# Kernel optimization log

Hardware: AMD Instinct MI355X
Metric: run time of the kernel (lower is better)

Reference implementation:

```python
import jax, jax.numpy as jnp
import numpy as np

# ---- fixed heterogeneous-graph metadata (Hetionet-like) ----
N_C, N_D, N_G = 15000, 3000, 40000          # Compound, Disease, Gene node counts
NODE_N = [N_C, N_D, N_G]
HID, OUT, HEADS, LAYERS = 128, 64, 4, 2
DH = HID // HEADS                            # 32 = head dim
# edge types as (src_type, dst_type):
#  0 treats C->D, 1 rev_treats D->C, 2 binds C->G, 3 rev_binds G->C, 4 interacts G->G
EDGE_META = [(0, 1), (1, 0), (0, 2), (2, 0), (2, 2)]
E_CNT = [80000, 80000, 250000, 250000, 400000]
N_EDGE_TYPES = len(EDGE_META)
N_ADD = 8000                                 # int(n_train * ratio * (epoch-1)) = int(80000*0.05*2)


def setup_inputs() -> dict:
    key = jax.random.key(0)
    ks = iter(jax.random.split(key, 64))
    s = 0.05
    inp = {}
    # node-type embedding tables (the model uses embed.weight as input features)
    inp['emb_compound'] = jax.random.normal(next(ks), (N_C, HID), jnp.float32) * s
    inp['emb_disease'] = jax.random.normal(next(ks), (N_D, HID), jnp.float32) * s
    inp['emb_gene'] = jax.random.normal(next(ks), (N_G, HID), jnp.float32) * s
    # HGTConv params, stacked over [layer, node_type] / [layer, edge_type]
    inp['W_kqv'] = jax.random.normal(next(ks), (LAYERS, 3, HID, 3 * HID), jnp.float32) * s
    inp['b_kqv'] = jnp.zeros((LAYERS, 3, 3 * HID), jnp.float32)
    inp['W_out'] = jax.random.normal(next(ks), (LAYERS, 3, HID, HID), jnp.float32) * s
    inp['b_out'] = jnp.zeros((LAYERS, 3, HID), jnp.float32)
    inp['skip'] = jnp.ones((LAYERS, 3), jnp.float32)
    inp['a_rel'] = jax.random.normal(next(ks), (LAYERS, N_EDGE_TYPES, HEADS, DH, DH), jnp.float32) * s
    inp['m_rel'] = jax.random.normal(next(ks), (LAYERS, N_EDGE_TYPES, HEADS, DH, DH), jnp.float32) * s
    inp['p_rel'] = jnp.ones((LAYERS, N_EDGE_TYPES, HEADS), jnp.float32)
    # final per-node-type Linear(hidden -> out)
    inp['W_fin'] = jax.random.normal(next(ks), (3, HID, OUT), jnp.float32) * s
    inp['b_fin'] = jnp.zeros((3, OUT), jnp.float32)
    # edge indices per edge type: [2, E] with row0=src idx, row1=dst idx
    names = ['ei_treats', 'ei_rev_treats', 'ei_binds', 'ei_rev_binds', 'ei_interacts']
    for name, (st, dt), e in zip(names, EDGE_META, E_CNT):
        src = jax.random.randint(next(ks), (e,), 0, NODE_N[st], dtype=jnp.int32)
        dst = jax.random.randint(next(ks), (e,), 0, NODE_N[dt], dtype=jnp.int32)
        inp[name] = jnp.stack([src, dst], 0)
    inp['train_edge_index'] = inp['ei_treats']
    inp['n_edge_add'] = int(N_ADD)
    return inp


def _hgt_layer(x_list, edge_list, Wkqv, bkqv, Wout, bout, skip, a_rel, m_rel, p_rel):
    """One PyG-style HGTConv layer over the heterogeneous graph."""
    kqv = [x @ Wkqv[t] + bkqv[t] for t, x in enumerate(x_list)]
    k = [a[:, :HID].reshape(-1, HEADS, DH) for a in kqv]
    q = [a[:, HID:2 * HID].reshape(-1, HEADS, DH) for a in kqv]
    v = [a[:, 2 * HID:].reshape(-1, HEADS, DH) for a in kqv]
    scale = 1.0 / np.sqrt(DH)
    buf = {t: {'a': [], 'v': [], 'i': []} for t in range(3)}
    for e, (st, dt) in enumerate(EDGE_META):
        src, dst = edge_list[e][0], edge_list[e][1]
        # per-edge-type, per-head relation transforms of gathered src k/v
        k_e = jnp.einsum('ehd,hdf->ehf', k[st][src], a_rel[e])   # [E,H,DH]
        v_e = jnp.einsum('ehd,hdf->ehf', v[st][src], m_rel[e])   # [E,H,DH]
        alpha = (q[dt][dst] * k_e).sum(-1) * p_rel[e] * scale    # [E,H]
        buf[dt]['a'].append(alpha); buf[dt]['v'].append(v_e); buf[dt]['i'].append(dst)
    out_list = []
    for t, x in enumerate(x_list):
        n = NODE_N[t]
        alpha = jnp.concatenate(buf[t]['a'], 0)
        vv = jnp.concatenate(buf[t]['v'], 0)
        idx = jnp.concatenate(buf[t]['i'], 0)
        # softmax over all incoming edges per destination node (across edge types)
        m = jax.ops.segment_max(alpha, idx, num_segments=n)
        ex = jnp.exp(alpha - m[idx])
        den = jax.ops.segment_sum(ex, idx, num_segments=n)
        w = ex / (den[idx] + 1e-16)
        agg = jax.ops.segment_sum(w[:, :, None] * vv, idx, num_segments=n).reshape(n, HID)
        o = jax.nn.gelu(agg, approximate=False) @ Wout[t] + bout[t]
        a_s = jax.nn.sigmoid(skip[t])
        out_list.append(a_s * o + (1.0 - a_s) * x)
    return out_list


def reference(emb_compound, emb_disease, emb_gene, W_kqv, b_kqv, W_out, b_out, skip,
              a_rel, m_rel, p_rel, W_fin, b_fin,
              ei_treats, ei_rev_treats, ei_binds, ei_rev_binds, ei_interacts,
              train_edge_index, n_edge_add):
    edge_list = [ei_treats, ei_rev_treats, ei_binds, ei_rev_binds, ei_interacts]
    # encode: embeddings -> HGT convs -> per-type linear
    x = [emb_compound, emb_disease, emb_gene]
    for l in range(LAYERS):
        x = _hgt_layer(x, edge_list, W_kqv[l], b_kqv[l], W_out[l], b_out[l],
                       skip[l], a_rel[l], m_rel[l], p_rel[l])
    z = [x[t] @ W_fin[t] + b_fin[t] for t in range(3)]
    # decode_all: dense prob matrix, zero out training edges, global top-k
    prob = jax.nn.sigmoid(z[0] @ z[1].T)                     # [N_C, N_D]
    prob = prob.at[train_edge_index[0], train_edge_index[1]].set(0.0)
    _, top_idx = jax.lax.top_k(prob.reshape(-1), n_edge_add)
    row = top_idx // N_D
    col = top_idx % N_D
    edge_index_add = jnp.stack([row, col], 0)
    edge_weight_add = prob[row, col]
    return edge_index_add, edge_weight_add
```

## Files before the change

### kernel.cpp

```cpp
#include <hip/hip_runtime.h>
#include <hip/hip_bf16.h>
#include <math.h>

#define N_C 15000
#define N_D 3000
#define N_G 40000
#define NTOT 58000
#define HID 128
#define HEADS 4
#define DH 32
#define KTOP 8000
#define KROWP 3072
#define NPROBP 46202880u
#define EQCAP 1048576u
#define DPB 8
#define EPB 8

#define SC_DEN 1125899906842624.0
#define SC_AGG 281474976710656.0

static __device__ __forceinline__ unsigned fenc32(float f){
    unsigned u = __float_as_uint(f);
    return (u & 0x80000000u) ? ~u : (u | 0x80000000u);
}
static __device__ __forceinline__ float fdec32(unsigned um){
    return __uint_as_float((um & 0x80000000u) ? (um & 0x7fffffffu) : ~um);
}

static __device__ __forceinline__ float pexp32f(float x){
    x = fminf(x,  88.3762626647949f);
    x = fmaxf(x, -87.3365478515625f);
    float fx = fmaf(x, 1.44269504088896341f, 0.5f);
    fx = floorf(fx);
    float r = fmaf(fx, -0.693359375f, x);
    r = fmaf(fx, 2.12194440e-4f, r);
    float r2 = __fmul_rn(r, r);
    float y = 1.9875691500E-4f;
    y = fmaf(y, r, 1.3981999507E-3f);
    y = fmaf(y, r, 8.3334519073E-3f);
    y = fmaf(y, r, 4.1665795894E-2f);
    y = fmaf(y, r, 1.6666665459E-1f);
    y = fmaf(y, r, 5.0000001201E-1f);
    y = fmaf(y, r2, r);
    y = __fadd_rn(y, 1.0f);
    int m = (int)fx;
    y = __fmul_rn(y, __uint_as_float((unsigned)(m + 127) << 23));
    return y;
}

static __device__ __forceinline__ float np_sigmoid_f32(float x){
    float e = pexp32f(-x);
    float s = __fadd_rn(1.0f, e);
    return __fdiv_rn(1.0f, s);
}

__global__ void k_init_nmax(unsigned* __restrict__ NMAX){
    int i = blockIdx.x*256 + threadIdx.x;
    if (i < NTOT*HEADS) NMAX[i] = 0x007FFFFFu;
}

__global__ void k_count(const int* __restrict__ edst, unsigned* __restrict__ cnt, int E){
    int i = blockIdx.x*256 + threadIdx.x;
    if (i < E) atomicAdd(&cnt[edst[i]], 1u);
}

__global__ void __launch_bounds__(256) k_scan(const unsigned* __restrict__ cnt,
                                              unsigned* __restrict__ offs, int n){
    __shared__ unsigned ssum[256];
    int tid = threadIdx.x;
    int chunk = (n + 255) / 256;
    int lo = tid*chunk, hi = lo+chunk; if (hi > n) hi = n; if (lo > n) lo = n;
    unsigned s = 0;
    for (int i=lo;i<hi;i++) s += cnt[i];
    ssum[tid] = s; __syncthreads();
    for (int st=1; st<256; st<<=1){
        unsigned t = (tid>=st) ? ssum[tid-st] : 0u;
        __syncthreads();
        ssum[tid] += t;
        __syncthreads();
    }
    unsigned run = ssum[tid] - s;
    for (int i=lo;i<hi;i++){ offs[i] = run; run += cnt[i]; }
    if (tid == 0) offs[n] = ssum[255];
}

__global__ void k_fill(const int* __restrict__ esrc, const int* __restrict__ edst,
                       const unsigned* __restrict__ offs, unsigned* __restrict__ curs,
                       unsigned* __restrict__ csr_src, unsigned* __restrict__ csr_el,
                       int E, int csr_base){
    int i = blockIdx.x*256 + threadIdx.x;
    if (i >= E) return;
    int dst = edst[i];
    unsigned pos = offs[dst] + atomicAdd(&curs[dst], 1u);
    csr_src[csr_base + pos] = (unsigned)esrc[i];
    csr_el [csr_base + pos] = (unsigned)i;
}

__global__ void k_kqv(const float* __restrict__ X, const float* __restrict__ W,
                      const float* __restrict__ Bv, float* __restrict__ KQ,
                      float* __restrict__ V, int n0, int ncnt)
{
    __shared__ float sA[16][128];
    int rb = blockIdx.x*16;
    int sec = blockIdx.y;
    int col = threadIdx.x & 127, half = threadIdx.x >> 7;
    for (int i = threadIdx.x; i < 2048; i += 256){
        int r = i >> 7, c = i & 127;
        sA[r][c] = (rb + r < ncnt) ? X[(size_t)(n0+rb+r)*HID + c] : 0.f;
    }
    __syncthreads();
    float acc[8];
#pragma unroll
    for (int i=0;i<8;i++) acc[i]=0.f;
    int wc = sec*128 + col;
    for (int k=0;k<128;k++){
        float w = W[(size_t)k*384 + wc];
#pragma unroll
        for (int i=0;i<8;i++) acc[i] = fmaf(sA[half*8+i][k], w, acc[i]);
    }
    float bb = Bv[wc];
    for (int i=0;i<8;i++){
        int r = rb + half*8 + i;
        if (r >= ncnt) continue;
        float y = __fadd_rn(acc[i], bb);
        if (sec < 2) KQ[(size_t)(n0+r)*256 + sec*128 + col] = y;
        else         V[(size_t)(n0+r)*128 + col] = y;
    }
}

__global__ void __launch_bounds__(256) k_rel(const float* __restrict__ IN, int stride, int secoff,
        const float* __restrict__ Mrel, float* __restrict__ OUT, int n0, int ncnt)
{
    __shared__ float sM[HEADS*DH*DH];
    for (int i=threadIdx.x;i<HEADS*DH*DH;i+=256) sM[i]=Mrel[i];
    __syncthreads();
    int sub = threadIdx.x>>7, lane = threadIdx.x&127;
    int h = lane>>5, f = lane&31;
    int row = blockIdx.x*2 + sub;
    if (row >= ncnt) return;
    float vval = IN[(size_t)(n0+row)*stride + secoff + lane];
    double t = 0.0;
    const float* mh = &sM[h*DH*DH];
#pragma unroll
    for (int d=0; d<DH; ++d)
        t += (double)__shfl(vval, d, 32) * (double)mh[d*DH+f];
    OUT[(size_t)row*HID + lane] = (float)t;
}

__global__ void __launch_bounds__(256) k_alpha4(const float* __restrict__ KQ,
        const float* __restrict__ KE,
        const int* __restrict__ esrc, const int* __restrict__ edst,
        const float* __restrict__ Prel,
        float* __restrict__ ALPHA, unsigned* __restrict__ NMAX,
        int E, int eoff, int nodst)
{
    int sub = threadIdx.x>>7, lane = threadIdx.x&127;
    int h = lane>>5, f = lane&31;
    float p = Prel[h];
    int ebase = (blockIdx.x*2 + sub) * EPB;
#pragma unroll
    for (int i=0;i<EPB;i++){
        int e = ebase + i;
        if (e >= E) return;
        int src = esrc[e], dst = edst[e];
        float ke = KE[(size_t)src*HID + lane];
        float qv = KQ[(size_t)(nodst+dst)*256 + 128 + lane];
        double part = (double)qv * (double)ke;
#pragma unroll
        for (int off=16; off>0; off>>=1) part += __shfl_xor(part, off);
        if (f==0){
            float s32 = (float)part;
            float a = __fmul_rn(__fmul_rn(s32, p), 0.17677669529663687f);
            ALPHA[(size_t)(eoff+e)*HEADS + h] = a;
            atomicMax(&NMAX[(size_t)(nodst+dst)*HEADS + h], fenc32(a));
        }
    }
}

__global__ void k_expsum(const float* __restrict__ ALPHA,
                         const int* __restrict__ edst, const unsigned* __restrict__ NMAX,
                         unsigned long long* __restrict__ NSUM,
                         int E, int eoff, int nodst)
{
    int i = blockIdx.x*256 + threadIdx.x;
    if (i >= E*HEADS) return;
    int e = i>>2, h = i&3;
    int dst = edst[e];
    float m = fdec32(NMAX[(size_t)(nodst+dst)*HEADS + h]);
    float a = ALPHA[(size_t)(eoff+e)*HEADS + h];
    float ex = pexp32f(__fsub_rn(a, m));
    atomicAdd(&NSUM[(size_t)(nodst+dst)*HEADS + h],
              (unsigned long long)(long long)llrint((double)ex * SC_DEN));
}

__global__ void k_den(const unsigned long long* __restrict__ NSUM, float* __restrict__ DEN){
    int i = blockIdx.x*256 + threadIdx.x;
    if (i >= NTOT*HEADS) return;
    DEN[i] = (float)((double)(long long)NSUM[i] * (1.0/SC_DEN));
}

__global__ void k_wgt(float* __restrict__ ALPHA, const int* __restrict__ edst,
                      const unsigned* __restrict__ NMAX, const float* __restrict__ DEN,
                      int E, int eoff, int nodst)
{
    int i = blockIdx.x*256 + threadIdx.x;
    if (i >= E*HEADS) return;
    int e = i>>2, h = i&3;
    int dst = edst[e];
    float m = fdec32(NMAX[(size_t)(nodst+dst)*HEADS + h]);
    float a = ALPHA[(size_t)(eoff+e)*HEADS + h];
    float ex = pexp32f(__fsub_rn(a, m));
    float denp = __fadd_rn(DEN[(size_t)(nodst+dst)*HEADS + h], 1e-16f);
    ALPHA[(size_t)(eoff+e)*HEADS + h] = __fdiv_rn(ex, denp);
}

__global__ void __launch_bounds__(128) k_agg2(
    const float* __restrict__ VE, const unsigned* __restrict__ csr_src,
    const unsigned* __restrict__ csr_el, const unsigned* __restrict__ offs,
    const float* __restrict__ W, unsigned long long* __restrict__ AGG,
    int eoff, int nodst, int csr_base, int ndst)
{
    int lane = threadIdx.x, h = lane>>5;
    int d0 = blockIdx.x*DPB;
    int d1 = d0+DPB; if (d1 > ndst) d1 = ndst;
    for (int dst=d0; dst<d1; ++dst){
        unsigned beg = offs[dst], end = offs[dst+1];
        if (beg == end) continue;
        long long acc = 0;
        for (unsigned j=beg; j<end; ++j){
            unsigned src = csr_src[csr_base+j];
            unsigned el  = csr_el [csr_base+j];
            float w  = W[(size_t)(eoff+el)*HEADS + h];
            float ve = VE[(size_t)src*HID + lane];
            float prod = __fmul_rn(w, ve);
            acc += llrint((double)prod*SC_AGG);
        }
        size_t o = (size_t)(nodst+dst)*HID + lane;
        AGG[o] = AGG[o] + (unsigned long long)acc;
    }
}

__global__ void k_outl(const unsigned long long* __restrict__ AGG,
                       const float* __restrict__ W, const float* __restrict__ Bv,
                       float* __restrict__ X,
                       const float* __restrict__ skipv, int n0, int ncnt)
{
    __shared__ float sA[16][128];
    int rb = blockIdx.x*16;
    int col = threadIdx.x&127, half = threadIdx.x>>7;
    for (int i=threadIdx.x;i<2048;i+=256){
        int r=i>>7,c=i&127;
        float g = 0.f;
        if (rb+r<ncnt){
            float x = (float)((double)(long long)AGG[(size_t)(n0+rb+r)*128 + c] * (1.0/SC_AGG));
            float t = __fdiv_rn(x, 1.4142135623730951f);
            float ef = (float)erf((double)t);
            g = __fmul_rn(__fmul_rn(0.5f, x), __fadd_rn(1.0f, ef));
        }
        sA[r][c]=g;
    }
    __syncthreads();
    float acc[8];
#pragma unroll
    for(int i=0;i<8;i++)acc[i]=0.f;
    for(int k=0;k<128;k++){
        float w=W[(size_t)k*128+col];
#pragma unroll
        for(int i=0;i<8;i++)acc[i]=fmaf(sA[half*8+i][k], w, acc[i]);
    }
    float a_s = np_sigmoid_f32(skipv[0]);
    float om  = __fsub_rn(1.0f, a_s);
    for(int i=0;i<8;i++){
        int r=rb+half*8+i;
        if(r<ncnt){
            size_t idx=(size_t)(n0+r)*128+col;
            float o = __fadd_rn(acc[i], Bv[col]);
            X[idx] = __fadd_rn(__fmul_rn(a_s, o), __fmul_rn(om, X[idx]));
        }
    }
}

__global__ void k_zfin(const float* __restrict__ X, const float* __restrict__ W,
                       const float* __restrict__ Bv, float* __restrict__ Z,
                       int n0, int ncnt, int zoff)
{
    __shared__ float sA[16][128];
    int rb=blockIdx.x*16;
    int col=threadIdx.x&63, quad=threadIdx.x>>6;
    for(int i=threadIdx.x;i<2048;i+=256){
        int r=i>>7,c=i&127;
        sA[r][c]=(rb+r<ncnt)?X[(size_t)(n0+rb+r)*128+c]:0.f;
    }
    __syncthreads();
    float acc[4]={0.f,0.f,0.f,0.f};
    for(int k=0;k<128;k++){
        float w=W[(size_t)k*64+col];
#pragma unroll
        for(int i=0;i<4;i++)acc[i]=fmaf(sA[quad*4+i][k], w, acc[i]);
    }
    for(int i=0;i<4;i++){
        int r=rb+quad*4+i;
        if(r<ncnt)Z[(size_t)(zoff+r)*64+col]=__fadd_rn(acc[i], Bv[col]);
    }
}

__global__ void k_mask(const int* __restrict__ tr, unsigned* __restrict__ MASK, int E){
    int i = blockIdx.x*256 + threadIdx.x;
    if (i>=E) return;
    unsigned bit = (unsigned)(tr[i]*KROWP + tr[E+i]);
    atomicOr(&MASK[bit>>5], 1u<<(bit&31));
}

__global__ void __launch_bounds__(256) k_keys(const float* __restrict__ Z,
        const unsigned* __restrict__ MASK, unsigned* __restrict__ KEYS,
        unsigned* __restrict__ STATE)
{
    __shared__ float sC[64][65];
    __shared__ float sD[64][65];
    __shared__ unsigned shh[256];
    int db = blockIdx.x*64, cb = blockIdx.y*64;
    shh[threadIdx.x] = 0u;
    for (int i=threadIdx.x;i<4096;i+=256){
        int r=i>>6, c=i&63;
        sC[r][c] = (cb+r<N_C) ? Z[(size_t)(cb+r)*64+c] : 0.f;
        sD[r][c] = (db+r<N_D) ? Z[(size_t)(N_C+db+r)*64+c] : 0.f;
    }
    __syncthreads();
    int tx = threadIdx.x & 15, ty = threadIdx.x >> 4;
    int r0 = ty*4, c0 = tx*4;
    float acc[4][4];
#pragma unroll
    for(int i=0;i<4;i++)
#pragma unroll
        for(int j=0;j<4;j++) acc[i][j]=0.f;
    for (int k=0;k<64;k++){
        float a0=sC[r0][k],a1=sC[r0+1][k],a2=sC[r0+2][k],a3=sC[r0+3][k];
        float b0=sD[c0][k],b1=sD[c0+1][k],b2=sD[c0+2][k],b3=sD[c0+3][k];
        acc[0][0]=fmaf(a0,b0,acc[0][0]); acc[0][1]=fmaf(a0,b1,acc[0][1]);
        acc[0][2]=fmaf(a0,b2,acc[0][2]); acc[0][3]=fmaf(a0,b3,acc[0][3]);
        acc[1][0]=fmaf(a1,b0,acc[1][0]); acc[1][1]=fmaf(a1,b1,acc[1][1]);
        acc[1][2]=fmaf(a1,b2,acc[1][2]); acc[1][3]=fmaf(a1,b3,acc[1][3]);
        acc[2][0]=fmaf(a2,b0,acc[2][0]); acc[2][1]=fmaf(a2,b1,acc[2][1]);
        acc[2][2]=fmaf(a2,b2,acc[2][2]); acc[2][3]=fmaf(a2,b3,acc[2][3]);
        acc[3][0]=fmaf(a3,b0,acc[3][0]); acc[3][1]=fmaf(a3,b1,acc[3][1]);
        acc[3][2]=fmaf(a3,b2,acc[3][2]); acc[3][3]=fmaf(a3,b3,acc[3][3]);
    }
    unsigned lastb=0xFFFFFFFFu, rcnt=0;
#pragma unroll
    for (int i=0;i<4;i++){
        int cr = cb + r0 + i;
        int dcb = db + c0;
        bool rok = (cr < N_C);
        unsigned mword = rok ? MASK[((size_t)cr*KROWP + dcb)>>5] : 0u;
        unsigned kk[4];
#pragma unroll
        for (int j=0;j<4;j++){
            int dc = dcb + j;
            unsigned key = 0u;
            if (rok && dc < N_D){
                float p = np_sigmoid_f32(acc[i][j]);
                key = fenc32(p);
                if (mword & (1u << (dc & 31))) key = 0u;
            }
            kk[j] = key;
            unsigned b = key >> 24;
            if (b == lastb) rcnt++;
            else { if (rcnt) atomicAdd(&shh[lastb], rcnt); lastb = b; rcnt = 1; }
        }
        *reinterpret_cast<uint4*>(&KEYS[(size_t)cr*KROWP + dcb]) =
            make_uint4(kk[0],kk[1],kk[2],kk[3]);
    }
    if (rcnt) atomicAdd(&shh[lastb], rcnt);
    __syncthreads();
    unsigned v = shh[threadIdx.x];
    if (v) atomicAdd(&STATE[8+threadIdx.x], v);
}

__global__ void k_hist(const unsigned* __restrict__ KEYS, unsigned* __restrict__ STATE, int level){
    __shared__ unsigned sh[256];
    for (int i=threadIdx.x;i<256;i+=blockDim.x) sh[i]=0;
    __syncthreads();
    unsigned prefix = STATE[0];
    int shift = 24 - 8*level;
    size_t stride = (size_t)gridDim.x*blockDim.x;
    unsigned lastb = 0xFFFFFFFFu, rcnt = 0;
    for (size_t i = (size_t)blockIdx.x*blockDim.x+threadIdx.x; i < (size_t)NPROBP; i += stride){
        unsigned k = KEYS[i];
        if ((k >> (shift+8)) != prefix) continue;
        unsigned b = (k>>shift)&255u;
        if (b == lastb) rcnt++;
        else { if (rcnt) atomicAdd(&sh[lastb], rcnt); lastb = b; rcnt = 1; }
    }
    if (rcnt) atomicAdd(&sh[lastb], rcnt);
    __syncthreads();
    for (int i=threadIdx.x;i<256;i+=blockDim.x) if (sh[i]) atomicAdd(&STATE[8+i], sh[i]);
}

__global__ void k_hfin(unsigned* STATE){
    if (threadIdx.x==0 && blockIdx.x==0){
        unsigned cnt = STATE[1];
        unsigned prefix = STATE[0];
        int b = 255;
        for (; b>0; --b){
            unsigned c = STATE[8+b];
            if (cnt + c >= (unsigned)KTOP) break;
            cnt += c;
        }
        STATE[0] = (prefix<<8) | (unsigned)b;
        STATE[1] = cnt;
        for (int i=0;i<256;i++) STATE[8+i]=0;
    }
}

__global__ void k_collect(const unsigned* __restrict__ KEYS, unsigned* __restrict__ STATE,
                          unsigned long long* __restrict__ CANDI, unsigned* __restrict__ EQI)
{
    unsigned T = STATE[0];
    size_t stride = (size_t)gridDim.x*blockDim.x;
    for (size_t i=(size_t)blockIdx.x*blockDim.x+threadIdx.x; i<(size_t)NPROBP; i+=stride){
        unsigned k = KEYS[i];
        if (k > T){
            unsigned pos = atomicAdd(&STATE[2], 1u);
            if (pos < 8192u)
                CANDI[pos] = ((unsigned long long)k << 32)
                           | (unsigned long long)(0xFFFFFFFFu - (unsigned)i);
        } else if (k == T){
            unsigned pos = atomicAdd(&STATE[3], 1u);
            if (pos < EQCAP) EQI[pos] = (unsigned)i;
        }
    }
}

__global__ void __launch_bounds__(1024) k_exact(const unsigned long long* __restrict__ CANDI,
        const unsigned* __restrict__ STATE, const unsigned* __restrict__ EQI,
        float* __restrict__ OUT)
{
    __shared__ unsigned long long s[8192];
    unsigned* si = (unsigned*)s;
    unsigned G = STATE[2]; if (G > 8192u) G = 8192u;
    unsigned nE = STATE[3]; if (nE > EQCAP) nE = EQCAP;
    unsigned T = STATE[0];
    unsigned gEmit = (G < (unsigned)KTOP) ? G : (unsigned)KTOP;

    for (unsigned i=threadIdx.x; i<8192u; i+=1024u)
        s[i] = (i < G) ? CANDI[i] : 0ull;
    __syncthreads();
    for(int k2=2;k2<=8192;k2<<=1){
      for(int j=k2>>1;j>0;j>>=1){
        for(int t=threadIdx.x;t<8192;t+=1024){
            int ixj=t^j;
            if(ixj>t){
                unsigned long long a=s[t],b=s[ixj];
                bool desc=((t&k2)==0);
                if(desc?(a<b):(a>b)){s[t]=b;s[ixj]=a;}
            }
        }
        __syncthreads();
      }
    }
    for (unsigned r=threadIdx.x; r<gEmit; r+=1024u){
        unsigned long long v = s[r];
        unsigned idx = 0xFFFFFFFFu - (unsigned)(v & 0xFFFFFFFFull);
        unsigned key = (unsigned)(v >> 32);
        unsigned c = idx/KROWP, d = idx - c*KROWP;
        OUT[r] = (float)c; OUT[KTOP+r] = (float)d; OUT[2*KTOP+r] = fdec32(key);
    }
    __syncthreads();

    if (G < (unsigned)KTOP){
        float pT = fdec32(T);
        for (unsigned i=threadIdx.x; i<8192u; i+=1024u)
            si[i] = (i < nE) ? EQI[i] : 0xFFFFFFFFu;
        __syncthreads();
        for(int k2=2;k2<=8192;k2<<=1){
          for(int j=k2>>1;j>0;j>>=1){
            for(int t=threadIdx.x;t<8192;t+=1024){
                int ixj=t^j;
                if(ixj>t){
                    unsigned a=si[t],b=si[ixj];
                    bool asc=((t&k2)==0);
                    if(asc?(a>b):(a<b)){si[t]=b;si[ixj]=a;}
                }
            }
            __syncthreads();
          }
        }
        unsigned need = (unsigned)KTOP - G;
        for (unsigned r=threadIdx.x; r<need; r+=1024u){
            unsigned idx = si[r];
            unsigned c = idx/KROWP, d = idx - c*KROWP;
            unsigned rr = G + r;
            OUT[rr] = (float)c; OUT[KTOP+rr] = (float)d; OUT[2*KTOP+rr] = pT;
        }
    }
}

extern "C" void kernel_launch(void* const* d_in, const int* in_sizes, int n_in,
                              void* d_out, int out_size, void* d_ws, size_t ws_size,
                              hipStream_t stream)
{
    const float* embC = (const float*)d_in[0];
    const float* embD = (const float*)d_in[1];
    const float* embG = (const float*)d_in[2];
    const float* Wkqv = (const float*)d_in[3];
    const float* bkqv = (const float*)d_in[4];
    const float* Wout = (const float*)d_in[5];
    const float* bout = (const float*)d_in[6];
    const float* skipv= (const float*)d_in[7];
    const float* arel = (const float*)d_in[8];
    const float* mrel = (const float*)d_in[9];
    const float* prel = (const float*)d_in[10];
    const float* Wfin = (const float*)d_in[11];
    const float* bfin = (const float*)d_in[12];
    const int* ei[5] = {(const int*)d_in[13],(const int*)d_in[14],(const int*)d_in[15],
                        (const int*)d_in[16],(const int*)d_in[17]};
    const int* tri  = (const int*)d_in[18];
    int trE = in_sizes[18]/2;

    static const int NODE_OFF[3] = {0, N_C, N_C + N_D};
    static const int NODE_CNT[3] = {N_C, N_D, N_G};
    static const int EM_ST[5] = {0,1,0,2,2};
    static const int EM_DT[5] = {1,0,2,0,2};
    static const int EM_E[5]  = {80000,80000,250000,250000,400000};
    static const int EM_OFF[5]= {0,80000,160000,410000,660000};
    static const int DOFF[5] = {0,3000,18000,58000,73000};
    static const int OFO[5]  = {0,3001,18002,58003,73004};

    char* ws = (char*)d_ws;
    float* X  = (float*)(ws + 0);
    float* KQ = (float*)(ws + 29696000);
    float* V  = (float*)(ws + 89088000);
    float* ALPHA = (float*)(ws + 118784000);
    unsigned* NMAX = (unsigned*)(ws + 135744000);
    unsigned long long* NSUM = (unsigned long long*)(ws + 136672000);
    float* DEN = (float*)(ws + 138528000);
    unsigned long long* AGG = (unsigned long long*)(ws + 139456000);
    float* VE = (float*)(ws + 198848000);
    unsigned* OFFS = (unsigned*)(ws + 219328000);
    unsigned* CURS = (unsigned*)(ws + 219780032);
    unsigned* CSRS = (unsigned*)(ws + 220232032);
    unsigned* CSRE = (unsigned*)(ws + 224472032);
    float* KE = (float*)(ws + 228712032);
    unsigned* KEYS = (unsigned*)(ws + 0);
    float* Z = (float*)(ws + 198848000);
    unsigned* MASK = (unsigned*)(ws + 203456000);
    unsigned* STATE= (unsigned*)(ws + 209216000);
    unsigned long long* CANDI = (unsigned long long*)(ws + 209224192);
    unsigned* EQI  = (unsigned*)(ws + 209289728);

    hipMemcpyAsync(X,                          embC, (size_t)N_C*HID*4, hipMemcpyDeviceToDevice, stream);
    hipMemcpyAsync(X + (size_t)N_C*HID,        embD, (size_t)N_D*HID*4, hipMemcpyDeviceToDevice, stream);
    hipMemcpyAsync(X + (size_t)(N_C+N_D)*HID,  embG, (size_t)N_G*HID*4, hipMemcpyDeviceToDevice, stream);

    hipMemsetAsync(CURS, 0, 113000*4, stream);
    for (int e=0;e<5;e++)
        k_count<<<(EM_E[e]+255)/256, 256, 0, stream>>>(ei[e]+EM_E[e], CURS + DOFF[e], EM_E[e]);
    for (int e=0;e<5;e++)
        k_scan<<<1, 256, 0, stream>>>(CURS + DOFF[e], OFFS + OFO[e], NODE_CNT[EM_DT[e]]);
    hipMemsetAsync(CURS, 0, 113000*4, stream);
    for (int e=0;e<5;e++)
        k_fill<<<(EM_E[e]+255)/256, 256, 0, stream>>>(ei[e], ei[e]+EM_E[e],
            OFFS + OFO[e], CURS + DOFF[e], CSRS, CSRE, EM_E[e], EM_OFF[e]);

    for (int l=0; l<2; ++l){
        k_init_nmax<<<(NTOT*HEADS+255)/256, 256, 0, stream>>>(NMAX);
        hipMemsetAsync(NSUM, 0, (size_t)NTOT*HEADS*8, stream);
        hipMemsetAsync(AGG,  0, (size_t)NTOT*HID*8,  stream);
        for (int t=0;t<3;t++){
            k_kqv<<<dim3((NODE_CNT[t]+15)/16, 3), 256, 0, stream>>>(
                X, Wkqv + (size_t)(l*3+t)*128*384, bkqv + (size_t)(l*3+t)*384,
                KQ, V, NODE_OFF[t], NODE_CNT[t]);
        }
        for (int e=0;e<5;e++){
            int nsrc = NODE_CNT[EM_ST[e]];
            k_rel<<<(nsrc+1)/2, 256, 0, stream>>>(
                KQ, 256, 0, arel + (size_t)(l*5+e)*HEADS*DH*DH, KE,
                NODE_OFF[EM_ST[e]], nsrc);
            int ngrp = (EM_E[e] + EPB - 1) / EPB;
            k_alpha4<<<(ngrp+1)/2, 256, 0, stream>>>(
                KQ, KE, ei[e], ei[e]+EM_E[e],
                prel + (size_t)(l*5+e)*HEADS,
                ALPHA, NMAX, EM_E[e], EM_OFF[e], NODE_OFF[EM_DT[e]]);
        }
        for (int e=0;e<5;e++){
            int tot = EM_E[e]*HEADS;
            k_expsum<<<(tot+255)/256, 256, 0, stream>>>(
                ALPHA, ei[e]+EM_E[e], NMAX, NSUM, EM_E[e], EM_OFF[e], NODE_OFF[EM_DT[e]]);
        }
        k_den<<<(NTOT*HEADS+255)/256, 256, 0, stream>>>(NSUM, DEN);
        for (int e=0;e<5;e++){
            int tot = EM_E[e]*HEADS;
            k_wgt<<<(tot+255)/256, 256, 0, stream>>>(
                ALPHA, ei[e]+EM_E[e], NMAX, DEN, EM_E[e], EM_OFF[e], NODE_OFF[EM_DT[e]]);
        }
        for (int e=0;e<5;e++){
            int nsrc = NODE_CNT[EM_ST[e]];
            int ndst = NODE_CNT[EM_DT[e]];
            k_rel<<<(nsrc+1)/2, 256, 0, stream>>>(
                V, 128, 0, mrel + (size_t)(l*5+e)*HEADS*DH*DH, VE,
                NODE_OFF[EM_ST[e]], nsrc);
            k_agg2<<<(ndst+DPB-1)/DPB, 128, 0, stream>>>(
                VE, CSRS, CSRE, OFFS + OFO[e], ALPHA, AGG,
                EM_OFF[e], NODE_OFF[EM_DT[e]], EM_OFF[e], ndst);
        }
        for (int t=0;t<3;t++){
            k_outl<<<(NODE_CNT[t]+15)/16, 256, 0, stream>>>(
                AGG, Wout + (size_t)(l*3+t)*128*128, bout + (size_t)(l*3+t)*128,
                X, skipv + (l*3+t), NODE_OFF[t], NODE_CNT[t]);
        }
    }

    k_zfin<<<(N_C+15)/16, 256, 0, stream>>>(X, Wfin + 0,      bfin + 0,  Z, 0,   N_C, 0);
    k_zfin<<<(N_D+15)/16, 256, 0, stream>>>(X, Wfin + 128*64, bfin + 64, Z, N_C, N_D, N_C);

    hipMemsetAsync(MASK, 0, 5760000, stream);
    hipMemsetAsync(STATE, 0, 8192, stream);
    k_mask<<<(trE+255)/256, 256, 0, stream>>>(tri, MASK, trE);
    k_keys<<<dim3(48, 235), 256, 0, stream>>>(Z, MASK, KEYS, STATE);
    k_hfin<<<1, 64, 0, stream>>>(STATE);
    for (int lev=1; lev<4; ++lev){
        k_hist<<<2048, 256, 0, stream>>>(KEYS, STATE, lev);
        k_hfin<<<1, 64, 0, stream>>>(STATE);
    }
    k_collect<<<2048, 256, 0, stream>>>(KEYS, STATE, CANDI, EQI);
    k_exact<<<1, 1024, 0, stream>>>(CANDI, STATE, EQI, (float*)d_out);
}
```

Measured before the change: 3.567 ms.

## Use CSR-ordered alpha kernel, fold den into wgt, parallel rank-based top-k emit

The attention-score kernel now walks destinations through the CSR instead of the raw edge list. It keeps a per-destination running max so only one atomicMax is issued per destination and head, and the query vector is reused across incoming edges. The separate denominator kernel is removed and k_wgt converts NSUM inline. The single-block bitonic sort of the final candidates is replaced by a 64-block counting-rank kernel that computes each element's output position by comparing against all candidates. This caps equal-key ties at 8192 instead of EQCAP, and it relies on the CSR element-index mapping holding the original edge ids.

```diff
diff --git a/kernel.cpp b/kernel.cpp
--- a/kernel.cpp
+++ b/kernel.cpp
@@ -14,7 +14,6 @@
 #define NPROBP 46202880u
 #define EQCAP 1048576u
 #define DPB 8
-#define EPB 8
 
 #define SC_DEN 1125899906842624.0
 #define SC_AGG 281474976710656.0
@@ -147,33 +146,38 @@
     OUT[(size_t)row*HID + lane] = (float)t;
 }
 
-__global__ void __launch_bounds__(256) k_alpha4(const float* __restrict__ KQ,
+__global__ void __launch_bounds__(128) k_alpha_csr(const float* __restrict__ KQ,
         const float* __restrict__ KE,
-        const int* __restrict__ esrc, const int* __restrict__ edst,
-        const float* __restrict__ Prel,
+        const unsigned* __restrict__ csr_src, const unsigned* __restrict__ csr_el,
+        const unsigned* __restrict__ offs, const float* __restrict__ Prel,
         float* __restrict__ ALPHA, unsigned* __restrict__ NMAX,
-        int E, int eoff, int nodst)
-{
-    int sub = threadIdx.x>>7, lane = threadIdx.x&127;
-    int h = lane>>5, f = lane&31;
+        int eoff, int nodst, int csr_base, int ndst)
+{
+    int lane = threadIdx.x, h = lane>>5, f = lane&31;
     float p = Prel[h];
-    int ebase = (blockIdx.x*2 + sub) * EPB;
-#pragma unroll
-    for (int i=0;i<EPB;i++){
-        int e = ebase + i;
-        if (e >= E) return;
-        int src = esrc[e], dst = edst[e];
-        float ke = KE[(size_t)src*HID + lane];
+    int d0 = blockIdx.x*DPB;
+    int d1 = d0+DPB; if (d1 > ndst) d1 = ndst;
+    for (int dst=d0; dst<d1; ++dst){
+        unsigned beg = offs[dst], end = offs[dst+1];
+        if (beg == end) continue;
         float qv = KQ[(size_t)(nodst+dst)*256 + 128 + lane];
-        double part = (double)qv * (double)ke;
-#pragma unroll
-        for (int off=16; off>0; off>>=1) part += __shfl_xor(part, off);
-        if (f==0){
-            float s32 = (float)part;
-            float a = __fmul_rn(__fmul_rn(s32, p), 0.17677669529663687f);
-            ALPHA[(size_t)(eoff+e)*HEADS + h] = a;
-            atomicMax(&NMAX[(size_t)(nodst+dst)*HEADS + h], fenc32(a));
-        }
+        unsigned lmax = 0x007FFFFFu;
+        for (unsigned j=beg; j<end; ++j){
+            unsigned src = csr_src[csr_base+j];
+            unsigned el  = csr_el [csr_base+j];
+            float ke = KE[(size_t)src*HID + lane];
+            double part = (double)qv * (double)ke;
+#pragma unroll
+            for (int off=16; off>0; off>>=1) part += __shfl_xor(part, off);
+            if (f==0){
+                float s32 = (float)part;
+                float a = __fmul_rn(__fmul_rn(s32, p), 0.17677669529663687f);
+                ALPHA[(size_t)(eoff+el)*HEADS + h] = a;
+                unsigned enc = fenc32(a);
+                if (enc > lmax) lmax = enc;
+            }
+        }
+        if (f==0) atomicMax(&NMAX[(size_t)(nodst+dst)*HEADS + h], lmax);
     }
 }
 
@@ -193,14 +197,9 @@
               (unsigned long long)(long long)llrint((double)ex * SC_DEN));
 }
 
-__global__ void k_den(const unsigned long long* __restrict__ NSUM, float* __restrict__ DEN){
-    int i = blockIdx.x*256 + threadIdx.x;
-    if (i >= NTOT*HEADS) return;
-    DEN[i] = (float)((double)(long long)NSUM[i] * (1.0/SC_DEN));
-}
-
 __global__ void k_wgt(float* __restrict__ ALPHA, const int* __restrict__ edst,
-                      const unsigned* __restrict__ NMAX, const float* __restrict__ DEN,
+                      const unsigned* __restrict__ NMAX,
+                      const unsigned long long* __restrict__ NSUM,
                       int E, int eoff, int nodst)
 {
     int i = blockIdx.x*256 + threadIdx.x;
@@ -210,7 +209,8 @@
     float m = fdec32(NMAX[(size_t)(nodst+dst)*HEADS + h]);
     float a = ALPHA[(size_t)(eoff+e)*HEADS + h];
     float ex = pexp32f(__fsub_rn(a, m));
-    float denp = __fadd_rn(DEN[(size_t)(nodst+dst)*HEADS + h], 1e-16f);
+    float den = (float)((double)(long long)NSUM[(size_t)(nodst+dst)*HEADS + h] * (1.0/SC_DEN));
+    float denp = __fadd_rn(den, 1e-16f);
     ALPHA[(size_t)(eoff+e)*HEADS + h] = __fdiv_rn(ex, denp);
 }
 
@@ -431,65 +431,51 @@
     }
 }
 
-__global__ void __launch_bounds__(1024) k_exact(const unsigned long long* __restrict__ CANDI,
+__global__ void __launch_bounds__(256) k_rank(const unsigned long long* __restrict__ CANDI,
         const unsigned* __restrict__ STATE, const unsigned* __restrict__ EQI,
         float* __restrict__ OUT)
 {
-    __shared__ unsigned long long s[8192];
-    unsigned* si = (unsigned*)s;
+    __shared__ unsigned long long sc[2048];
+    unsigned* se = (unsigned*)sc;
     unsigned G = STATE[2]; if (G > 8192u) G = 8192u;
-    unsigned nE = STATE[3]; if (nE > EQCAP) nE = EQCAP;
+    unsigned nE = STATE[3]; if (nE > 8192u) nE = 8192u;
     unsigned T = STATE[0];
-    unsigned gEmit = (G < (unsigned)KTOP) ? G : (unsigned)KTOP;
-
-    for (unsigned i=threadIdx.x; i<8192u; i+=1024u)
-        s[i] = (i < G) ? CANDI[i] : 0ull;
-    __syncthreads();
-    for(int k2=2;k2<=8192;k2<<=1){
-      for(int j=k2>>1;j>0;j>>=1){
-        for(int t=threadIdx.x;t<8192;t+=1024){
-            int ixj=t^j;
-            if(ixj>t){
-                unsigned long long a=s[t],b=s[ixj];
-                bool desc=((t&k2)==0);
-                if(desc?(a<b):(a>b)){s[t]=b;s[ixj]=a;}
-            }
-        }
-        __syncthreads();
-      }
-    }
-    for (unsigned r=threadIdx.x; r<gEmit; r+=1024u){
-        unsigned long long v = s[r];
-        unsigned idx = 0xFFFFFFFFu - (unsigned)(v & 0xFFFFFFFFull);
-        unsigned key = (unsigned)(v >> 32);
-        unsigned c = idx/KROWP, d = idx - c*KROWP;
-        OUT[r] = (float)c; OUT[KTOP+r] = (float)d; OUT[2*KTOP+r] = fdec32(key);
-    }
-    __syncthreads();
-
-    if (G < (unsigned)KTOP){
+    unsigned need = ((unsigned)KTOP > G) ? ((unsigned)KTOP - G) : 0u;
+
+    int phase = blockIdx.x & 1;
+    unsigned i = (blockIdx.x >> 1)*256 + threadIdx.x;
+    if (phase == 0){
+        unsigned long long ci = (i < G) ? CANDI[i] : 0ull;
+        unsigned rank = 0;
+        for (unsigned t0=0; t0<G; t0+=2048u){
+            unsigned tl = G - t0; if (tl > 2048u) tl = 2048u;
+            __syncthreads();
+            for (unsigned k=threadIdx.x; k<tl; k+=256u) sc[k] = CANDI[t0+k];
+            __syncthreads();
+            if (i < G)
+                for (unsigned k=0; k<tl; ++k) rank += (sc[k] > ci) ? 1u : 0u;
+        }
+        if (i < G){
+            unsigned idx = 0xFFFFFFFFu - (unsigned)(ci & 0xFFFFFFFFull);
+            unsigned key = (unsigned)(ci >> 32);
+            unsigned c = idx/KROWP, d = idx - c*KROWP;
+            OUT[rank] = (float)c; OUT[KTOP+rank] = (float)d; OUT[2*KTOP+rank] = fdec32(key);
+        }
+    } else {
         float pT = fdec32(T);
-        for (unsigned i=threadIdx.x; i<8192u; i+=1024u)
-            si[i] = (i < nE) ? EQI[i] : 0xFFFFFFFFu;
-        __syncthreads();
-        for(int k2=2;k2<=8192;k2<<=1){
-          for(int j=k2>>1;j>0;j>>=1){
-            for(int t=threadIdx.x;t<8192;t+=1024){
-                int ixj=t^j;
-                if(ixj>t){
-                    unsigned a=si[t],b=si[ixj];
-                    bool asc=((t&k2)==0);
-                    if(asc?(a>b):(a<b)){si[t]=b;si[ixj]=a;}
-                }
-            }
+        unsigned ii = (i < nE) ? EQI[i] : 0xFFFFFFFFu;
+        unsigned rank = 0;
+        for (unsigned t0=0; t0<nE; t0+=2048u){
+            unsigned tl = nE - t0; if (tl > 2048u) tl = 2048u;
             __syncthreads();
-          }
-        }
-        unsigned need = (unsigned)KTOP - G;
-        for (unsigned r=threadIdx.x; r<need; r+=1024u){
-            unsigned idx = si[r];
-            unsigned c = idx/KROWP, d = idx - c*KROWP;
-            unsigned rr = G + r;
+            for (unsigned k=threadIdx.x; k<tl; k+=256u) se[k] = EQI[t0+k];
+            __syncthreads();
+            if (i < nE)
+                for (unsigned k=0; k<tl; ++k) rank += (se[k] < ii) ? 1u : 0u;
+        }
+        if (i < nE && rank < need){
+            unsigned c = ii/KROWP, d = ii - c*KROWP;
+            unsigned rr = G + rank;
             OUT[rr] = (float)c; OUT[KTOP+rr] = (float)d; OUT[2*KTOP+rr] = pT;
         }
     }
@@ -533,7 +519,6 @@
     float* ALPHA = (float*)(ws + 118784000);
     unsigned* NMAX = (unsigned*)(ws + 135744000);
     unsigned long long* NSUM = (unsigned long long*)(ws + 136672000);
-    float* DEN = (float*)(ws + 138528000);
     unsigned long long* AGG = (unsigned long long*)(ws + 139456000);
     float* VE = (float*)(ws + 198848000);
     unsigned* OFFS = (unsigned*)(ws + 219328000);
@@ -573,25 +558,24 @@
         }
         for (int e=0;e<5;e++){
             int nsrc = NODE_CNT[EM_ST[e]];
+            int ndst = NODE_CNT[EM_DT[e]];
             k_rel<<<(nsrc+1)/2, 256, 0, stream>>>(
                 KQ, 256, 0, arel + (size_t)(l*5+e)*HEADS*DH*DH, KE,
                 NODE_OFF[EM_ST[e]], nsrc);
-            int ngrp = (EM_E[e] + EPB - 1) / EPB;
-            k_alpha4<<<(ngrp+1)/2, 256, 0, stream>>>(
-                KQ, KE, ei[e], ei[e]+EM_E[e],
+            k_alpha_csr<<<(ndst+DPB-1)/DPB, 128, 0, stream>>>(
+                KQ, KE, CSRS, CSRE, OFFS + OFO[e],
                 prel + (size_t)(l*5+e)*HEADS,
-                ALPHA, NMAX, EM_E[e], EM_OFF[e], NODE_OFF[EM_DT[e]]);
+                ALPHA, NMAX, EM_OFF[e], NODE_OFF[EM_DT[e]], EM_OFF[e], ndst);
         }
         for (int e=0;e<5;e++){
             int tot = EM_E[e]*HEADS;
             k_expsum<<<(tot+255)/256, 256, 0, stream>>>(
                 ALPHA, ei[e]+EM_E[e], NMAX, NSUM, EM_E[e], EM_OFF[e], NODE_OFF[EM_DT[e]]);
         }
-        k_den<<<(NTOT*HEADS+255)/256, 256, 0, stream>>>(NSUM, DEN);
         for (int e=0;e<5;e++){
             int tot = EM_E[e]*HEADS;
             k_wgt<<<(tot+255)/256, 256, 0, stream>>>(
-                ALPHA, ei[e]+EM_E[e], NMAX, DEN, EM_E[e], EM_OFF[e], NODE_OFF[EM_DT[e]]);
+                ALPHA, ei[e]+EM_E[e], NMAX, NSUM, EM_E[e], EM_OFF[e], NODE_OFF[EM_DT[e]]);
         }
         for (int e=0;e<5;e++){
             int nsrc = NODE_CNT[EM_ST[e]];
@@ -623,5 +607,5 @@
         k_hfin<<<1, 64, 0, stream>>>(STATE);
     }
     k_collect<<<2048, 256, 0, stream>>>(KEYS, STATE, CANDI, EQI);
-    k_exact<<<1, 1024, 0, stream>>>(CANDI, STATE, EQI, (float*)d_out);
-}
+    k_rank<<<64, 256, 0, stream>>>(CANDI, STATE, EQI, (float*)d_out);
+}
```

New measurement: 3.791 ms. +6.3%, slower.
